# Optimization experiments

Measured on AMD Instinct MI355X. Metric: run time of the kernel, lower is better.

## Reference

```python
import jax, jax.numpy as jnp
import numpy as np

B, H, W, CIN, COUT, KH, KW = 16, 64, 64, 256, 256, 3, 3


def setup_inputs() -> dict:
    key = jax.random.key(0)
    k1, k2, k3 = jax.random.split(key, 3)
    x = jax.random.normal(k1, (B, H, W, CIN), dtype=jnp.float32)
    style = jax.random.normal(k2, (B, CIN), dtype=jnp.float32)
    # glorot-ish scale for the base kernel
    kernel = jax.random.normal(k3, (KH, KW, CIN, COUT), dtype=jnp.float32) * 0.05
    return {"x": x, "style": style, "kernel": kernel}


def reference(x, style, kernel):
    b = x.shape[0]
    cout = kernel.shape[-1]
    # Modulate: per-sample weights [B, kh, kw, Cin, Cout]
    w = kernel[None] * (style[:, None, None, :, None] + 1.0)
    # Demodulate: L2 normalize over (kh, kw, Cin) per (sample, out-channel)
    w = w / jnp.sqrt(jnp.sum(jnp.square(w), axis=(1, 2, 3), keepdims=True) + 1e-8)
    # Batch-as-groups grouped conv: x -> [1, B*Cin, H, W]
    xg = jnp.transpose(x, (0, 3, 1, 2)).reshape(1, -1, x.shape[1], x.shape[2])
    # w -> [kh, kw, Cin, B*Cout]
    wg = jnp.transpose(w, (1, 2, 3, 0, 4)).reshape(w.shape[1], w.shape[2], w.shape[3], -1)
    y = jax.lax.conv_general_dilated(
        xg, wg,
        window_strides=(1, 1),
        padding='SAME',
        dimension_numbers=('NCHW', 'HWIO', 'NCHW'),
        feature_group_count=b,
    )
    # [1, B*Cout, H, W] -> [B, H, W, Cout]
    y = y.reshape(b, cout, y.shape[2], y.shape[3])
    return jnp.transpose(y, (0, 2, 3, 1))
```

## Files before the change

kernel.cpp:

```cpp
#include <hip/hip_runtime.h>


#define HH 64
#define WW 64
#define CI 256
#define CO 256
#define KTOT 2304
#define CIPITCH 40
#define XCOLS 66
#define BPITCH 100

typedef float    f32x4 __attribute__((ext_vector_type(4)));
typedef _Float16 f16x8 __attribute__((ext_vector_type(8)));
typedef __fp16   fp16x2 __attribute__((ext_vector_type(2)));

__device__ __forceinline__ unsigned pk2(float a, float b) {
    fp16x2 h = __builtin_amdgcn_cvt_pkrtz(a, b);
    return __builtin_bit_cast(unsigned, h);
}

__global__ __launch_bounds__(256) void prep(
    const float* __restrict__ kern,
    const float* __restrict__ style,
    ushort* __restrict__ Wt,
    float* __restrict__ scale2)
{
    __shared__ ushort tile[64][65];
    __shared__ float  sqt[64][65];
    __shared__ float  st2l[16][64];

    const int kt = blockIdx.x >> 2;
    const int ct = blockIdx.x & 3;
    const int k0 = kt * 64, c0 = ct * 64;
    const int ci0 = k0 & 255;
    const int tid = threadIdx.x;
    const int r = tid >> 2, q = tid & 3;

    #pragma unroll
    for (int p = 0; p < 4; ++p) {
        const int i = p * 256 + tid;
        const int bb = i >> 6, rr = i & 63;
        const float s = style[bb * CI + ci0 + rr] + 1.0f;
        st2l[bb][rr] = s * s;
    }

    const float* src = kern + (size_t)(k0 + r) * CO + c0 + q * 16;
    #pragma unroll
    for (int j = 0; j < 16; ++j) {
        const float v = src[j];
        _Float16 h = (_Float16)v;
        tile[q * 16 + j][r] = __builtin_bit_cast(unsigned short, h);
        sqt[r][q * 16 + j] = v * v;
    }
    __syncthreads();

    ushort* dst = Wt + (size_t)(c0 + r) * KTOT + k0 + q * 16;
    #pragma unroll
    for (int j = 0; j < 16; ++j) dst[j] = tile[r][q * 16 + j];

    const int co = tid & 63;
    const int bq = tid >> 6;
    float acc[4] = {0.f, 0.f, 0.f, 0.f};
    #pragma unroll 4
    for (int rr = 0; rr < 64; ++rr) {
        const float s = sqt[rr][co];
        #pragma unroll
        for (int bb = 0; bb < 4; ++bb)
            acc[bb] += s * st2l[bq * 4 + bb][rr];
    }
    #pragma unroll
    for (int bb = 0; bb < 4; ++bb)
        atomicAdd(&scale2[(bq * 4 + bb) * CO + c0 + co], acc[bb]);
}

__global__ __launch_bounds__(256) void gemm_conv(
    const float* __restrict__ x,
    const ushort* __restrict__ Wt,
    const float* __restrict__ style,
    const float* __restrict__ scale2,
    float* __restrict__ y)
{
    __shared__ __align__(16) ushort xs[4 * XCOLS * CIPITCH];
    __shared__ __align__(16) ushort bs[128 * BPITCH];
    __shared__ float s_style[CI];

    const int tid  = threadIdx.x;
    const int lane = tid & 63;
    const int wave = tid >> 6;

    const int mtile = blockIdx.x >> 1;
    const int n0    = (blockIdx.x & 1) * 128;
    const int p0    = mtile * 128;
    const int b     = p0 >> 12;
    const int h0    = (p0 >> 6) & 63;

    s_style[tid] = style[b * CI + tid] + 1.0f;

    const int wm = (wave & 1) * 64;
    const int wn = (wave >> 1) * 64;
    const int fr = lane & 15;
    const int fq = lane >> 4;
    const int xlane = fr * CIPITCH + fq * 8;

    f32x4 acc[4][4] = {};

    for (int c = 0; c < 8; ++c) {
        __syncthreads();

        #pragma unroll
        for (int p = 0; p < 9; ++p) {
            const int task = p * 256 + tid;
            if (task < 2112) {
                const int rowcol = task >> 3;
                const int chunk  = task & 7;
                const int row = rowcol / XCOLS;
                const int col = rowcol - row * XCOLS;
                const int rg = h0 - 1 + row;
                const int cg = col - 1;
                f32x4 v = {0.f, 0.f, 0.f, 0.f};
                if ((unsigned)rg < 64u && (unsigned)cg < 64u)
                    v = *(const f32x4*)(x + ((size_t)((b * HH + rg) * WW + cg)) * CI
                                          + c * 32 + chunk * 4);
                const f32x4 st = *(const f32x4*)(s_style + c * 32 + chunk * 4);
                const f32x4 m = v * st;
                uint2 u;
                u.x = pk2(m.x, m.y);
                u.y = pk2(m.z, m.w);
                *(uint2*)(xs + rowcol * CIPITCH + chunk * 4) = u;
            }
        }

        #pragma unroll
        for (int tr = 0; tr < 3; ++tr) {
            if (tr) __syncthreads();

            #pragma unroll
            for (int p = 0; p < 6; ++p) {
                const int task = p * 256 + tid;
                const int co = task / 12;
                const int r  = task - co * 12;
                const int tl = r >> 2;
                const int ch = r & 3;
                const uint4 v = *(const uint4*)(Wt + (size_t)(n0 + co) * KTOT
                                                + (tr * 3 + tl) * 256 + c * 32 + ch * 8);
                *(uint4*)(bs + co * BPITCH + tl * 32 + ch * 8) = v;
            }
            __syncthreads();

            #pragma unroll
            for (int tl = 0; tl < 3; ++tl) {
                const int t  = tr * 3 + tl;
                const int dh = t / 3;
                const int dw = t - dh * 3;

                f16x8 af[4], bf[4];
                #pragma unroll
                for (int i = 0; i < 4; ++i) {
                    const int mb   = wm + i * 16;
                    const int mrow = (mb >> 6) + dh;
                    const int mcol = (mb & 63) + dw;
                    af[i] = *(const f16x8*)(xs + (mrow * XCOLS + mcol) * CIPITCH + xlane);
                }
                #pragma unroll
                for (int j = 0; j < 4; ++j)
                    bf[j] = *(const f16x8*)(bs + (wn + j * 16 + fr) * BPITCH
                                            + tl * 32 + fq * 8);
                #pragma unroll
                for (int i = 0; i < 4; ++i)
                    #pragma unroll
                    for (int j = 0; j < 4; ++j)
                        acc[i][j] = __builtin_amdgcn_mfma_f32_16x16x32_f16(
                            af[i], bf[j], acc[i][j], 0, 0, 0);
            }
        }
    }

    float sc[4];
    #pragma unroll
    for (int j = 0; j < 4; ++j)
        sc[j] = __frsqrt_rn(scale2[b * CO + n0 + wn + j * 16 + fr] + 1e-8f);
    #pragma unroll
    for (int i = 0; i < 4; ++i) {
        const int m_base = p0 + wm + i * 16 + fq * 4;
        #pragma unroll
        for (int j = 0; j < 4; ++j) {
            float* yp = y + (size_t)m_base * CO + n0 + wn + j * 16 + fr;
            #pragma unroll
            for (int r = 0; r < 4; ++r)
                yp[(size_t)r * CO] = acc[i][j][r] * sc[j];
        }
    }
}

extern "C" void kernel_launch(void* const* d_in, const int* in_sizes, int n_in,
                              void* d_out, int out_size, void* d_ws, size_t ws_size,
                              hipStream_t stream) {
    const float* x     = (const float*)d_in[0];
    const float* style = (const float*)d_in[1];
    const float* kern  = (const float*)d_in[2];
    float* out = (float*)d_out;

    float*  scale2 = (float*)d_ws;
    ushort* Wt     = (ushort*)((char*)d_ws + 16384);

    hipMemsetAsync(scale2, 0, 16 * CO * sizeof(float), stream);
    prep<<<144, 256, 0, stream>>>(kern, style, Wt, scale2);
    gemm_conv<<<512 * 2, 256, 0, stream>>>(x, Wt, style, scale2, out);
}
```

Before: 235.6 us.

## Prefetch weight tiles with async global_load_lds into triple-buffered LDS

The prep kernel now writes the fp16 weights in a layout tiled by (channel chunk, tap, k-quad, cout), so that each tap's B tile is one contiguous 8KB block per n-half. The GEMM loop loads these tiles directly into a three-slot LDS ring with global_load_lds, issued two taps ahead and gated by vmcnt waits and barriers, in place of synchronous register-staged copies. This is meant to hide weight-load latency behind the MFMA work and remove the padded-pitch staging. It relies on careful vmcnt accounting across the interleaved x loads, and LDS bank behaviour changes with the new unpadded layout.

Result: faster. 225.7 us (-4.2%).

```diff
diff --git a/kernel.cpp b/kernel.cpp
--- a/kernel.cpp
+++ b/kernel.cpp
@@ -8,7 +8,6 @@
 #define KTOT 2304
 #define CIPITCH 40
 #define XCOLS 66
-#define BPITCH 100
 
 typedef float    f32x4 __attribute__((ext_vector_type(4)));
 typedef _Float16 f16x8 __attribute__((ext_vector_type(8)));
@@ -22,7 +21,7 @@
 __global__ __launch_bounds__(256) void prep(
     const float* __restrict__ kern,
     const float* __restrict__ style,
-    ushort* __restrict__ Wt,
+    ushort* __restrict__ Wt2,
     float* __restrict__ scale2)
 {
     __shared__ ushort tile[64][65];
@@ -54,9 +53,18 @@
     }
     __syncthreads();
 
-    ushort* dst = Wt + (size_t)(c0 + r) * KTOT + k0 + q * 16;
-    #pragma unroll
-    for (int j = 0; j < 16; ++j) dst[j] = tile[r][q * 16 + j];
+    const int co_w = c0 + r;
+    #pragma unroll
+    for (int j = 0; j < 16; ++j) {
+        const int k   = k0 + q * 16 + j;
+        const int t9  = k >> 8;
+        const int rem = k & 255;
+        const int cc  = rem >> 5;
+        const int fq  = (rem >> 3) & 3;
+        const int e   = k & 7;
+        Wt2[((((size_t)cc * 9 + t9) * 4 + fq) * 256 + co_w) * 8 + e] =
+            tile[r][q * 16 + j];
+    }
 
     const int co = tid & 63;
     const int bq = tid >> 6;
@@ -75,13 +83,13 @@
 
 __global__ __launch_bounds__(256) void gemm_conv(
     const float* __restrict__ x,
-    const ushort* __restrict__ Wt,
+    const ushort* __restrict__ Wt2,
     const float* __restrict__ style,
     const float* __restrict__ scale2,
     float* __restrict__ y)
 {
     __shared__ __align__(16) ushort xs[4 * XCOLS * CIPITCH];
-    __shared__ __align__(16) ushort bs[128 * BPITCH];
+    __shared__ __align__(16) ushort bs[3 * 4096];
     __shared__ float s_style[CI];
 
     const int tid  = threadIdx.x;
@@ -102,56 +110,72 @@
     const int fq = lane >> 4;
     const int xlane = fr * CIPITCH + fq * 8;
 
+    auto issue_tile = [&](int cn, int t9n, int bufn) {
+        const ushort* gb = Wt2 + ((size_t)((cn * 9 + t9n) * 4) * 256 + n0) * 8;
+        #pragma unroll
+        for (int p = 0; p < 2; ++p) {
+            const int task = p * 256 + tid;
+            const ushort* g = gb + (size_t)(((task >> 7) << 8) + (task & 127)) * 8;
+            const ushort* l = bs + bufn * 4096 + (p * 256 + (tid & ~63)) * 8;
+            __builtin_amdgcn_global_load_lds(
+                (const __attribute__((address_space(1))) void*)g,
+                (__attribute__((address_space(3))) void*)l,
+                16, 0, 0);
+        }
+    };
+
     f32x4 acc[4][4] = {};
 
+    issue_tile(0, 0, 0);
+    issue_tile(0, 1, 1);
+
     for (int c = 0; c < 8; ++c) {
-        __syncthreads();
-
-        #pragma unroll
-        for (int p = 0; p < 9; ++p) {
-            const int task = p * 256 + tid;
-            if (task < 2112) {
-                const int rowcol = task >> 3;
-                const int chunk  = task & 7;
-                const int row = rowcol / XCOLS;
-                const int col = rowcol - row * XCOLS;
-                const int rg = h0 - 1 + row;
-                const int cg = col - 1;
-                f32x4 v = {0.f, 0.f, 0.f, 0.f};
-                if ((unsigned)rg < 64u && (unsigned)cg < 64u)
-                    v = *(const f32x4*)(x + ((size_t)((b * HH + rg) * WW + cg)) * CI
-                                          + c * 32 + chunk * 4);
-                const f32x4 st = *(const f32x4*)(s_style + c * 32 + chunk * 4);
-                const f32x4 m = v * st;
-                uint2 u;
-                u.x = pk2(m.x, m.y);
-                u.y = pk2(m.z, m.w);
-                *(uint2*)(xs + rowcol * CIPITCH + chunk * 4) = u;
+        #pragma unroll
+        for (int t9 = 0; t9 < 9; ++t9) {
+            asm volatile("s_waitcnt vmcnt(2) lgkmcnt(0)" ::: "memory");
+            __builtin_amdgcn_s_barrier();
+
+            if (t9 == 0) {
+                #pragma unroll
+                for (int p = 0; p < 9; ++p) {
+                    const int task = p * 256 + tid;
+                    if (task < 2112) {
+                        const int rowcol = task >> 3;
+                        const int chunk  = task & 7;
+                        const int row = rowcol / XCOLS;
+                        const int col = rowcol - row * XCOLS;
+                        const int rg = h0 - 1 + row;
+                        const int cg = col - 1;
+                        f32x4 v = {0.f, 0.f, 0.f, 0.f};
+                        if ((unsigned)rg < 64u && (unsigned)cg < 64u)
+                            v = *(const f32x4*)(x + ((size_t)((b * HH + rg) * WW + cg)) * CI
+                                                  + c * 32 + chunk * 4);
+                        const f32x4 st = *(const f32x4*)(s_style + c * 32 + chunk * 4);
+                        const f32x4 m = v * st;
+                        uint2 u;
+                        u.x = pk2(m.x, m.y);
+                        u.y = pk2(m.z, m.w);
+                        *(uint2*)(xs + rowcol * CIPITCH + chunk * 4) = u;
+                    }
+                }
+                asm volatile("s_waitcnt lgkmcnt(0)" ::: "memory");
+                __builtin_amdgcn_s_barrier();
             }
-        }
-
-        #pragma unroll
-        for (int tr = 0; tr < 3; ++tr) {
-            if (tr) __syncthreads();
-
-            #pragma unroll
-            for (int p = 0; p < 6; ++p) {
-                const int task = p * 256 + tid;
-                const int co = task / 12;
-                const int r  = task - co * 12;
-                const int tl = r >> 2;
-                const int ch = r & 3;
-                const uint4 v = *(const uint4*)(Wt + (size_t)(n0 + co) * KTOT
-                                                + (tr * 3 + tl) * 256 + c * 32 + ch * 8);
-                *(uint4*)(bs + co * BPITCH + tl * 32 + ch * 8) = v;
+
+            {
+                const int tn  = t9 + 2;
+                const int t9n = (tn >= 9) ? tn - 9 : tn;
+                if (t9 < 7) {
+                    issue_tile(c, t9n, t9n % 3);
+                } else if (c < 7) {
+                    issue_tile(c + 1, t9n, t9n % 3);
+                }
             }
-            __syncthreads();
-
-            #pragma unroll
-            for (int tl = 0; tl < 3; ++tl) {
-                const int t  = tr * 3 + tl;
-                const int dh = t / 3;
-                const int dw = t - dh * 3;
+
+            {
+                const int buf = t9 % 3;
+                const int dh  = t9 / 3;
+                const int dw  = t9 - dh * 3;
 
                 f16x8 af[4], bf[4];
                 #pragma unroll
@@ -163,8 +187,8 @@
                 }
                 #pragma unroll
                 for (int j = 0; j < 4; ++j)
-                    bf[j] = *(const f16x8*)(bs + (wn + j * 16 + fr) * BPITCH
-                                            + tl * 32 + fq * 8);
+                    bf[j] = *(const f16x8*)(bs + buf * 4096 + fq * 1024
+                                            + (wn + j * 16 + fr) * 8);
                 #pragma unroll
                 for (int i = 0; i < 4; ++i)
                     #pragma unroll
@@ -201,9 +225,9 @@
     float* out = (float*)d_out;
 
     float*  scale2 = (float*)d_ws;
-    ushort* Wt     = (ushort*)((char*)d_ws + 16384);
+    ushort* Wt2    = (ushort*)((char*)d_ws + 16384);
 
     hipMemsetAsync(scale2, 0, 16 * CO * sizeof(float), stream);
-    prep<<<144, 256, 0, stream>>>(kern, style, Wt, scale2);
-    gemm_conv<<<512 * 2, 256, 0, stream>>>(x, Wt, style, scale2, out);
-}
+    prep<<<144, 256, 0, stream>>>(kern, style, Wt2, scale2);
+    gemm_conv<<<512 * 2, 256, 0, stream>>>(x, Wt2, style, scale2, out);
+}
```
